# Optimization experiments

Measured on AMD Instinct MI355X. Metric: run time of the kernel, lower is better.

## Reference

```python
import jax, jax.numpy as jnp
import numpy as np

B, D, N, F = 2048, 512, 100000, 64
NEG = -1000000.0


def setup_inputs() -> dict:
    key = jax.random.key(0)
    k1, k2, k3, k4 = jax.random.split(key, 4)
    q = jax.random.normal(k1, (B, D), dtype=jnp.float32)
    rhs = jax.random.normal(k2, (D, N), dtype=jnp.float32)
    queries = jax.random.randint(k3, (B, 3), 0, N, dtype=jnp.int64)
    filter_idx = jax.random.randint(k4, (B, F), 0, N, dtype=jnp.int64)
    return {"q": q, "rhs": rhs, "queries": queries, "filter_idx": filter_idx}


def reference(q, rhs, queries, filter_idx):
    # targets[i] = score of the true triple = q[i] . rhs[:, true_rhs[i]]
    true_rhs = queries[:, 2]                         # [B]
    targets = jnp.einsum('bd,bd->b', q, rhs[:, true_rhs].T)  # [B]

    scores = q @ rhs                                  # [B, N]

    # filtered ranking: mask out known true tails + the query's own tail
    rows = jnp.arange(scores.shape[0])[:, None]       # [B, 1]
    scores = scores.at[rows, filter_idx].set(NEG)
    scores = scores.at[jnp.arange(scores.shape[0]), true_rhs].set(NEG)

    # rank = 1 + number of candidates scoring >= the true triple
    ranks = 1.0 + jnp.sum((scores >= targets[:, None]).astype(jnp.float32), axis=1)
    return ranks
```

## Files before the change

kernel.cpp:

```cpp
#include <hip/hip_runtime.h>
#include <hip/hip_bf16.h>

#define B_ 2048
#define D_ 512
#define N_ 100000
#define F_ 64
#define NEGV (-1000000.0f)

#define GEMM_BLKS 12512
#define TPOSE_BLKS 3125

typedef __bf16 bfx8 __attribute__((ext_vector_type(8)));
typedef float f32x4 __attribute__((ext_vector_type(4)));
typedef unsigned short u16x8 __attribute__((ext_vector_type(8)));

static __device__ __forceinline__ unsigned short f2bf(float f) {
  unsigned u = __float_as_uint(f);
  unsigned r = (u + 0x7fffu + ((u >> 16) & 1u)) >> 16;
  return (unsigned short)r;
}
static __device__ __forceinline__ float bf2f(unsigned short u) {
  return __uint_as_float(((unsigned)u) << 16);
}

static __device__ __forceinline__ void async_copy16(const void* g, void* l) {
  __builtin_amdgcn_global_load_lds((const __attribute__((address_space(1))) void*)g,
                                   (__attribute__((address_space(3))) void*)l, 16, 0, 0);
}

__global__ void prep(const float* __restrict__ q, const float* __restrict__ rhs,
                     const int* __restrict__ queries, float* __restrict__ targets,
                     float* __restrict__ out, unsigned short* __restrict__ qb,
                     unsigned short* __restrict__ rt) {
  __shared__ unsigned short obuf[32 * 512];
  __shared__ float wsum[4];
  int tid = threadIdx.x;

  if (blockIdx.x >= TPOSE_BLKS) {
    int b = blockIdx.x - TPOSE_BLKS;
    int lane = tid & 63, w = tid >> 6;
    int p = queries[b * 3 + 2];
    float2 v = ((const float2*)(q + (size_t)b * D_))[tid];
    ushort2 o; o.x = f2bf(v.x); o.y = f2bf(v.y);
    ((ushort2*)(qb + (size_t)b * D_))[tid] = o;
    float s = v.x * rhs[(size_t)(2 * tid) * N_ + p] + v.y * rhs[(size_t)(2 * tid + 1) * N_ + p];
    for (int off = 32; off; off >>= 1) s += __shfl_down(s, off, 64);
    if (lane == 0) wsum[w] = s;
    __syncthreads();
    if (tid == 0) {
      targets[b] = wsum[0] + wsum[1] + wsum[2] + wsum[3];
      out[b] = 1.0f;
    }
    return;
  }

  int n0 = blockIdx.x * 32;
  unsigned* ob32 = (unsigned*)obuf;
#pragma unroll
  for (int i = 0; i < 8; ++i) {
    int g = i * 256 + tid;
    int pd = g >> 3, c = g & 7;
    int d = pd * 2, n = c * 4;
    float4 v0 = *(const float4*)(rhs + (size_t)d * N_ + n0 + n);
    float4 v1 = *(const float4*)(rhs + (size_t)(d + 1) * N_ + n0 + n);
    const float* a0 = (const float*)&v0;
    const float* a1 = (const float*)&v1;
#pragma unroll
    for (int j = 0; j < 4; ++j) {
      unsigned pk = (unsigned)f2bf(a0[j]) | ((unsigned)f2bf(a1[j]) << 16);
      ob32[(n + j) * 256 + pd] = pk;
    }
  }
  __syncthreads();
  int w = tid >> 6, lane = tid & 63;
#pragma unroll
  for (int r = 0; r < 8; ++r) {
    int row = w * 8 + r;
    u16x8 val = *(const u16x8*)&obuf[row * 512 + lane * 8];
    *(u16x8*)(rt + (size_t)(n0 + row) * D_ + lane * 8) = val;
  }
}

__global__ void __launch_bounds__(256) gemm_corr(
    const unsigned short* __restrict__ qb,
    const unsigned short* __restrict__ rt,
    const int* __restrict__ queries,
    const int* __restrict__ filt,
    const float* __restrict__ targets,
    float* __restrict__ out) {
  __shared__ unsigned short As[2][128 * 32];
  __shared__ unsigned short Bs[2][128 * 32];
  __shared__ float sT[128];
  __shared__ int cnt2[2][128];
  __shared__ int idx[F_ + 1];
  __shared__ unsigned char uq[F_ + 1];

  int tid = threadIdx.x;
  int w = tid >> 6, lane = tid & 63;

  if (blockIdx.x < B_) {
    int b = blockIdx.x;
    if (tid <= F_) idx[tid] = (tid < F_) ? filt[b * F_ + tid] : queries[b * 3 + 2];
    __syncthreads();
    if (tid <= F_) {
      int p = idx[tid];
      bool u = true;
      for (int j = 0; j < tid; ++j)
        if (idx[j] == p) u = false;
      uq[tid] = u;
    }
    __syncthreads();
    float t = targets[b];
    float corr = 0.f;
    u16x8 qv = ((const u16x8*)(qb + (size_t)b * D_))[lane];
    for (int ii = w; ii <= F_; ii += 4) {
      if (!uq[ii]) continue;
      int p = idx[ii];
      u16x8 rv = ((const u16x8*)(rt + (size_t)p * D_))[lane];
      float s = 0.f;
#pragma unroll
      for (int j = 0; j < 8; ++j) s += bf2f(qv[j]) * bf2f(rv[j]);
      for (int off = 32; off; off >>= 1) s += __shfl_down(s, off, 64);
      if (lane == 0)
        corr += (NEGV >= t ? 1.f : 0.f) - (s >= t ? 1.f : 0.f);
    }
    if (lane == 0 && corr != 0.f) atomicAdd(&out[b], corr);
    return;
  }

  int g = blockIdx.x - B_;
  int lin = (g & 7) * (GEMM_BLKS / 8) + (g >> 3);
  int m0 = (lin & 15) * 128;
  int n0 = (lin >> 4) * 128;

  if (tid < 128) sT[tid] = targets[m0 + tid];

  int mw = (w & 1) * 64, nw = (w >> 1) * 64;
  int quad = lane >> 4, l16 = lane & 15;
  int xg = (quad ^ ((l16 >> 1) & 3)) * 8;

  int c0 = tid, c1 = 256 + tid;
  int am0 = c0 >> 2, am1 = c1 >> 2;
  int aj0 = ((c0 & 3) ^ ((c0 >> 3) & 3)) * 8;
  int aj1 = ((c1 & 3) ^ ((c1 >> 3) & 3)) * 8;
  int bn0g = n0 + am0; if (bn0g > N_ - 1) bn0g = N_ - 1;
  int bn1g = n0 + am1; if (bn1g > N_ - 1) bn1g = N_ - 1;
  const unsigned short* agp0 = qb + (size_t)(m0 + am0) * D_ + aj0;
  const unsigned short* agp1 = qb + (size_t)(m0 + am1) * D_ + aj1;
  const unsigned short* bgp0 = rt + (size_t)bn0g * D_ + aj0;
  const unsigned short* bgp1 = rt + (size_t)bn1g * D_ + aj1;

  f32x4 acc[4][4];
  f32x4 z = {0.f, 0.f, 0.f, 0.f};
#pragma unroll
  for (int i = 0; i < 4; ++i)
#pragma unroll
    for (int j = 0; j < 4; ++j) acc[i][j] = z;

  async_copy16(agp0, &As[0][c0 * 8]);
  async_copy16(agp1, &As[0][c1 * 8]);
  async_copy16(bgp0, &Bs[0][c0 * 8]);
  async_copy16(bgp1, &Bs[0][c1 * 8]);

  for (int kt = 0; kt < 16; ++kt) {
    int buf = kt & 1;
    __syncthreads();
    if (kt + 1 < 16) {
      int nb = 1 - buf, k1 = (kt + 1) * 32;
      async_copy16(agp0 + k1, &As[nb][c0 * 8]);
      async_copy16(agp1 + k1, &As[nb][c1 * 8]);
      async_copy16(bgp0 + k1, &Bs[nb][c0 * 8]);
      async_copy16(bgp1 + k1, &Bs[nb][c1 * 8]);
    }

    bfx8 a[4], b[4];
#pragma unroll
    for (int mi = 0; mi < 4; ++mi) {
      int m = mw + mi * 16 + l16;
      u16x8 au = *(const u16x8*)(&As[buf][m * 32 + xg]);
      a[mi] = __builtin_bit_cast(bfx8, au);
    }
#pragma unroll
    for (int ni = 0; ni < 4; ++ni) {
      int n = nw + ni * 16 + l16;
      u16x8 bu = *(const u16x8*)(&Bs[buf][n * 32 + xg]);
      b[ni] = __builtin_bit_cast(bfx8, bu);
    }
#pragma unroll
    for (int mi = 0; mi < 4; ++mi)
#pragma unroll
      for (int ni = 0; ni < 4; ++ni)
        acc[mi][ni] = __builtin_amdgcn_mfma_f32_16x16x32_bf16(a[mi], b[ni], acc[mi][ni], 0, 0, 0);
  }

#pragma unroll
  for (int mi = 0; mi < 4; ++mi) {
#pragma unroll
    for (int reg = 0; reg < 4; ++reg) {
      int rl = mw + mi * 16 + quad * 4 + reg;
      float t = sT[rl];
      int c = 0;
#pragma unroll
      for (int ni = 0; ni < 4; ++ni) {
        int col = n0 + nw + ni * 16 + l16;
        if (col < N_ && acc[mi][ni][reg] >= t) c++;
      }
      c += __shfl_xor(c, 1, 64);
      c += __shfl_xor(c, 2, 64);
      c += __shfl_xor(c, 4, 64);
      c += __shfl_xor(c, 8, 64);
      if (l16 == 0) cnt2[w >> 1][rl] = c;
    }
  }
  __syncthreads();
  if (tid < 128) {
    int tot = cnt2[0][tid] + cnt2[1][tid];
    if (tot) atomicAdd(&out[m0 + tid], (float)tot);
  }
}

__global__ void targets_init(const float* __restrict__ q, const float* __restrict__ rhs,
                             const int* __restrict__ queries, float* __restrict__ targets,
                             float* __restrict__ out) {
  __shared__ float wsum[4];
  int b = blockIdx.x;
  int tid = threadIdx.x, lane = tid & 63, w = tid >> 6;
  int p = queries[b * 3 + 2];
  float s = 0.f;
  for (int d = tid; d < D_; d += 256) s += q[b * D_ + d] * rhs[(size_t)d * N_ + p];
  for (int off = 32; off; off >>= 1) s += __shfl_down(s, off, 64);
  if (lane == 0) wsum[w] = s;
  __syncthreads();
  if (tid == 0) {
    targets[b] = wsum[0] + wsum[1] + wsum[2] + wsum[3];
    out[b] = 1.0f;
  }
}

__global__ void fallback_count(const float* __restrict__ q, const float* __restrict__ rhs,
                               const int* __restrict__ queries, const int* __restrict__ filt,
                               const float* __restrict__ targets, float* __restrict__ out) {
  int b = blockIdx.y;
  int n = blockIdx.x * 256 + threadIdx.x;
  __shared__ float qs[D_];
  __shared__ int idx[F_ + 1];
  __shared__ int cnt;
  for (int d = threadIdx.x; d < D_; d += 256) qs[d] = q[b * D_ + d];
  if (threadIdx.x < F_) idx[threadIdx.x] = filt[b * F_ + threadIdx.x];
  if (threadIdx.x == F_) idx[F_] = queries[b * 3 + 2];
  if (threadIdx.x == 0) cnt = 0;
  __syncthreads();
  if (n < N_) {
    float t = targets[b];
    float s = 0.f;
    for (int d = 0; d < D_; ++d) s += qs[d] * rhs[(size_t)d * N_ + n];
    bool member = false;
    for (int j = 0; j <= F_; ++j)
      if (idx[j] == n) member = true;
    float sv = member ? NEGV : s;
    if (sv >= t) atomicAdd(&cnt, 1);
  }
  __syncthreads();
  if (threadIdx.x == 0 && cnt) atomicAdd(&out[b], (float)cnt);
}

extern "C" void kernel_launch(void* const* d_in, const int* in_sizes, int n_in,
                              void* d_out, int out_size, void* d_ws, size_t ws_size,
                              hipStream_t stream) {
  const float* q = (const float*)d_in[0];
  const float* rhs = (const float*)d_in[1];
  const int* queries = (const int*)d_in[2];
  const int* filt = (const int*)d_in[3];
  float* out = (float*)d_out;

  char* wsb = (char*)d_ws;
  float* targets = (float*)wsb;
  unsigned short* qb = (unsigned short*)(wsb + 8192);
  unsigned short* rt = (unsigned short*)(wsb + 8192 + (size_t)B_ * D_ * 2);
  size_t need = 8192 + (size_t)B_ * D_ * 2 + (size_t)N_ * D_ * 2;

  if (ws_size >= need) {
    prep<<<TPOSE_BLKS + B_, 256, 0, stream>>>(q, rhs, queries, targets, out, qb, rt);
    gemm_corr<<<B_ + GEMM_BLKS, 256, 0, stream>>>(qb, rt, queries, filt, targets, out);
  } else {
    targets_init<<<B_, 256, 0, stream>>>(q, rhs, queries, targets, out);
    fallback_count<<<dim3((N_ + 255) / 256, B_), 256, 0, stream>>>(q, rhs, queries, filt, targets, out);
  }
}
```

Before: 603.0 us.

## Widen transpose tiles with swizzled LDS and split GEMM into two launches

The prep transpose now converts 64 columns per block instead of 32, clamps reads at the N boundary, and XOR-swizzles the LDS staging buffer to reduce bank conflicts on both the write and the read side. The GEMM grid is split into two launches of half the column tiles each, with the correction blocks only in the first, passing a column-tile base offset. The split adds a launch and a possible tail gap between kernels. The transpose change is meant to cut LDS conflicts and per-block overhead in the conversion pass.

```diff
diff --git a/kernel.cpp b/kernel.cpp
--- a/kernel.cpp
+++ b/kernel.cpp
@@ -7,8 +7,8 @@
 #define F_ 64
 #define NEGV (-1000000.0f)
 
-#define GEMM_BLKS 12512
-#define TPOSE_BLKS 3125
+#define GH 6256
+#define TP_BLKS 1563
 
 typedef __bf16 bfx8 __attribute__((ext_vector_type(8)));
 typedef float f32x4 __attribute__((ext_vector_type(4)));
@@ -32,12 +32,12 @@
                      const int* __restrict__ queries, float* __restrict__ targets,
                      float* __restrict__ out, unsigned short* __restrict__ qb,
                      unsigned short* __restrict__ rt) {
-  __shared__ unsigned short obuf[32 * 512];
+  __shared__ unsigned short obuf[64 * 512];
   __shared__ float wsum[4];
   int tid = threadIdx.x;
 
-  if (blockIdx.x >= TPOSE_BLKS) {
-    int b = blockIdx.x - TPOSE_BLKS;
+  if (blockIdx.x >= TP_BLKS) {
+    int b = blockIdx.x - TP_BLKS;
     int lane = tid & 63, w = tid >> 6;
     int p = queries[b * 3 + 2];
     float2 v = ((const float2*)(q + (size_t)b * D_))[tid];
@@ -54,30 +54,36 @@
     return;
   }
 
-  int n0 = blockIdx.x * 32;
+  int n0 = blockIdx.x * 64;
   unsigned* ob32 = (unsigned*)obuf;
 #pragma unroll
-  for (int i = 0; i < 8; ++i) {
-    int g = i * 256 + tid;
-    int pd = g >> 3, c = g & 7;
-    int d = pd * 2, n = c * 4;
-    float4 v0 = *(const float4*)(rhs + (size_t)d * N_ + n0 + n);
-    float4 v1 = *(const float4*)(rhs + (size_t)(d + 1) * N_ + n0 + n);
+  for (int i = 0; i < 16; ++i) {
+    int u = i * 256 + tid;
+    int dp = u >> 4, c4 = u & 15;
+    int cg = c4;
+    if (n0 + cg * 4 + 4 > N_) cg = (N_ - n0 - 4) >> 2;
+    int d = dp * 2;
+    float4 v0 = *(const float4*)(rhs + (size_t)d * N_ + n0 + cg * 4);
+    float4 v1 = *(const float4*)(rhs + (size_t)(d + 1) * N_ + n0 + cg * 4);
     const float* a0 = (const float*)&v0;
     const float* a1 = (const float*)&v1;
+    int sw = dp ^ ((c4 & 7) << 2);
 #pragma unroll
     for (int j = 0; j < 4; ++j) {
       unsigned pk = (unsigned)f2bf(a0[j]) | ((unsigned)f2bf(a1[j]) << 16);
-      ob32[(n + j) * 256 + pd] = pk;
+      ob32[(c4 * 4 + j) * 256 + sw] = pk;
     }
   }
   __syncthreads();
   int w = tid >> 6, lane = tid & 63;
 #pragma unroll
-  for (int r = 0; r < 8; ++r) {
-    int row = w * 8 + r;
-    u16x8 val = *(const u16x8*)&obuf[row * 512 + lane * 8];
-    *(u16x8*)(rt + (size_t)(n0 + row) * D_ + lane * 8) = val;
+  for (int r = 0; r < 16; ++r) {
+    int row = w * 16 + r;
+    if (n0 + row < N_) {
+      int lx = lane ^ ((row >> 2) & 7);
+      u16x8 val = *(const u16x8*)&ob32[row * 256 + lx * 4];
+      *(u16x8*)(rt + (size_t)(n0 + row) * D_ + lane * 8) = val;
+    }
   }
 }
 
@@ -87,7 +93,8 @@
     const int* __restrict__ queries,
     const int* __restrict__ filt,
     const float* __restrict__ targets,
-    float* __restrict__ out) {
+    float* __restrict__ out,
+    int pbase, int do_corr) {
   __shared__ unsigned short As[2][128 * 32];
   __shared__ unsigned short Bs[2][128 * 32];
   __shared__ float sT[128];
@@ -98,7 +105,7 @@
   int tid = threadIdx.x;
   int w = tid >> 6, lane = tid & 63;
 
-  if (blockIdx.x < B_) {
+  if (do_corr && blockIdx.x < B_) {
     int b = blockIdx.x;
     if (tid <= F_) idx[tid] = (tid < F_) ? filt[b * F_ + tid] : queries[b * 3 + 2];
     __syncthreads();
@@ -128,10 +135,10 @@
     return;
   }
 
-  int g = blockIdx.x - B_;
-  int lin = (g & 7) * (GEMM_BLKS / 8) + (g >> 3);
+  int g = blockIdx.x - (do_corr ? B_ : 0);
+  int lin = (g & 7) * (GH / 8) + (g >> 3);
   int m0 = (lin & 15) * 128;
-  int n0 = (lin >> 4) * 128;
+  int n0 = (pbase + (lin >> 4)) * 128;
 
   if (tid < 128) sT[tid] = targets[m0 + tid];
 
@@ -280,8 +287,9 @@
   size_t need = 8192 + (size_t)B_ * D_ * 2 + (size_t)N_ * D_ * 2;
 
   if (ws_size >= need) {
-    prep<<<TPOSE_BLKS + B_, 256, 0, stream>>>(q, rhs, queries, targets, out, qb, rt);
-    gemm_corr<<<B_ + GEMM_BLKS, 256, 0, stream>>>(qb, rt, queries, filt, targets, out);
+    prep<<<TP_BLKS + B_, 256, 0, stream>>>(q, rhs, queries, targets, out, qb, rt);
+    gemm_corr<<<B_ + GH, 256, 0, stream>>>(qb, rt, queries, filt, targets, out, 0, 1);
+    gemm_corr<<<GH, 256, 0, stream>>>(qb, rt, queries, filt, targets, out, 391, 0);
   } else {
     targets_init<<<B_, 256, 0, stream>>>(q, rhs, queries, targets, out);
     fallback_count<<<dim3((N_ + 255) / 256, B_), 256, 0, stream>>>(q, rhs, queries, filt, targets, out);
```

After: 610.5 us. No clear change (+1.2%).
